# Optimization experiments

Hardware: AMD Instinct MI355X
Metric: run time of the kernel (lower is better)

Reference implementation:

```python
import jax, jax.numpy as jnp
import numpy as np

B, T, H = 8, 4096, 1024

def setup_inputs() -> dict:
    key = jax.random.key(0)
    k1, k2, k3, k4 = jax.random.split(key, 4)
    states = jax.random.normal(k1, (B, T, H), dtype=jnp.float32)
    context = jax.random.normal(k2, (B, H), dtype=jnp.float32)
    # nn.Bilinear(H, H, 1): weight (1, H, H), bias (1,), init U(-1/sqrt(H), 1/sqrt(H))
    bound = 1.0 / np.sqrt(H)
    W = jax.random.uniform(k3, (1, H, H), dtype=jnp.float32, minval=-bound, maxval=bound)
    b = jax.random.uniform(k4, (1,), dtype=jnp.float32, minval=-bound, maxval=bound)
    return {"states": states, "context": context, "W": W, "b": b}

def reference(states, context, W, b):
    # score[b,t,0] = sum_{i,j} states[b,t,i] * W[0,i,j] * context[b,j] + b[0]
    # Algebraic rewrite: v[b,i] = sum_j W[0,i,j] * context[b,j]; score = states @ v + b
    v = jnp.einsum('ij,bj->bi', W[0], context)          # (B, H)
    scores = jnp.einsum('bti,bi->bt', states, v) + b[0]  # (B, T)
    return scores[..., None]                             # (B, T, 1)
```

## Files before the change

kernel.cpp:

```cpp
#include <hip/hip_runtime.h>


#define HDIM 1024
#define BDIM 8
#define TDIM 4096

typedef float v4f __attribute__((ext_vector_type(4)));

__global__ __launch_bounds__(256) void gs_compute_v(
    const float* __restrict__ W,
    const float* __restrict__ ctx,
    float* __restrict__ v)
{
    const int wave = (blockIdx.x << 2) | (threadIdx.x >> 6);
    const int lane = threadIdx.x & 63;
    const int i = wave >> 3;
    const int b = wave & 7;

    const v4f* __restrict__ Wrow = (const v4f*)(W + (size_t)i * HDIM);
    const v4f* __restrict__ Crow = (const v4f*)(ctx + (size_t)b * HDIM);

    float acc = 0.0f;
#pragma unroll
    for (int k = 0; k < 4; ++k) {
        v4f w4 = Wrow[k * 64 + lane];
        v4f c4 = Crow[k * 64 + lane];
        acc += w4.x * c4.x + w4.y * c4.y + w4.z * c4.z + w4.w * c4.w;
    }
#pragma unroll
    for (int off = 32; off > 0; off >>= 1)
        acc += __shfl_down(acc, off, 64);

    if (lane == 0) v[b * HDIM + i] = acc;
}

__global__ __launch_bounds__(256) void gs_compute_scores(
    const float* __restrict__ states,
    const float* __restrict__ v,
    const float* __restrict__ bias,
    float* __restrict__ out)
{
    const int row = (blockIdx.x << 2) | (threadIdx.x >> 6);
    const int lane = threadIdx.x & 63;
    const int b = row >> 12;

    const v4f* __restrict__ Srow = (const v4f*)(states + (size_t)row * HDIM);
    const v4f* __restrict__ Vrow = (const v4f*)(v + (size_t)b * HDIM);

    float acc = 0.0f;
#pragma unroll
    for (int k = 0; k < 4; ++k) {
        v4f s4 = __builtin_nontemporal_load(&Srow[k * 64 + lane]);
        v4f v4 = Vrow[k * 64 + lane];
        acc += s4.x * v4.x + s4.y * v4.y + s4.z * v4.z + s4.w * v4.w;
    }
#pragma unroll
    for (int off = 32; off > 0; off >>= 1)
        acc += __shfl_down(acc, off, 64);

    if (lane == 0) out[row] = acc + bias[0];
}

extern "C" void kernel_launch(void* const* d_in, const int* in_sizes, int n_in,
                              void* d_out, int out_size, void* d_ws, size_t ws_size,
                              hipStream_t stream)
{
    const float* states = (const float*)d_in[0];
    const float* ctx    = (const float*)d_in[1];
    const float* W      = (const float*)d_in[2];
    const float* bias   = (const float*)d_in[3];
    float* out = (float*)d_out;
    float* v   = (float*)d_ws;

    gs_compute_v<<<dim3((BDIM * HDIM) / 4), dim3(256), 0, stream>>>(W, ctx, v);
    gs_compute_scores<<<dim3((BDIM * TDIM) / 4), dim3(256), 0, stream>>>(states, v, bias, out);
}
```

Baseline: 186.4 us.

## Reuse W rows across batches and process multiple state rows per wave

The v kernel now has each wave handle one W row for all eight batch entries. W is read once instead of once per batch, at the cost of eight accumulators per lane. The scores kernel makes each wave process four consecutive rows and keeps the v slice and bias in registers. This cuts redundant v loads and launches fewer blocks, with more independent loads in flight per wave.

Measured after the change: 189.7 us. About the same (+1.8%).

```diff
diff --git a/kernel.cpp b/kernel.cpp
--- a/kernel.cpp
+++ b/kernel.cpp
@@ -4,6 +4,7 @@
 #define HDIM 1024
 #define BDIM 8
 #define TDIM 4096
+#define RPW  4
 
 typedef float v4f __attribute__((ext_vector_type(4)));
 
@@ -14,24 +15,36 @@
 {
     const int wave = (blockIdx.x << 2) | (threadIdx.x >> 6);
     const int lane = threadIdx.x & 63;
-    const int i = wave >> 3;
-    const int b = wave & 7;
 
-    const v4f* __restrict__ Wrow = (const v4f*)(W + (size_t)i * HDIM);
-    const v4f* __restrict__ Crow = (const v4f*)(ctx + (size_t)b * HDIM);
+    const v4f* __restrict__ Wrow = (const v4f*)(W + (size_t)wave * HDIM);
+    const v4f* __restrict__ C    = (const v4f*)ctx;
 
-    float acc = 0.0f;
+    float acc[BDIM];
+#pragma unroll
+    for (int b = 0; b < BDIM; ++b) acc[b] = 0.0f;
+
 #pragma unroll
     for (int k = 0; k < 4; ++k) {
         v4f w4 = Wrow[k * 64 + lane];
-        v4f c4 = Crow[k * 64 + lane];
-        acc += w4.x * c4.x + w4.y * c4.y + w4.z * c4.z + w4.w * c4.w;
+#pragma unroll
+        for (int b = 0; b < BDIM; ++b) {
+            v4f c4 = C[b * (HDIM / 4) + k * 64 + lane];
+            acc[b] += w4.x * c4.x + w4.y * c4.y + w4.z * c4.z + w4.w * c4.w;
+        }
     }
+
 #pragma unroll
-    for (int off = 32; off > 0; off >>= 1)
-        acc += __shfl_down(acc, off, 64);
+    for (int b = 0; b < BDIM; ++b) {
+#pragma unroll
+        for (int off = 32; off > 0; off >>= 1)
+            acc[b] += __shfl_down(acc[b], off, 64);
+    }
 
-    if (lane == 0) v[b * HDIM + i] = acc;
+    if (lane == 0) {
+#pragma unroll
+        for (int b = 0; b < BDIM; ++b)
+            v[b * HDIM + wave] = acc[b];
+    }
 }
 
 __global__ __launch_bounds__(256) void gs_compute_scores(
@@ -40,25 +53,37 @@
     const float* __restrict__ bias,
     float* __restrict__ out)
 {
-    const int row = (blockIdx.x << 2) | (threadIdx.x >> 6);
+    const int wave = (blockIdx.x << 2) | (threadIdx.x >> 6);
     const int lane = threadIdx.x & 63;
-    const int b = row >> 12;
+    const int row0 = wave * RPW;
+    const int b = row0 >> 12;
 
-    const v4f* __restrict__ Srow = (const v4f*)(states + (size_t)row * HDIM);
-    const v4f* __restrict__ Vrow = (const v4f*)(v + (size_t)b * HDIM);
+    const v4f* __restrict__ V = (const v4f*)(v + (size_t)b * HDIM);
+    const v4f vr0 = V[0 * 64 + lane];
+    const v4f vr1 = V[1 * 64 + lane];
+    const v4f vr2 = V[2 * 64 + lane];
+    const v4f vr3 = V[3 * 64 + lane];
+    const float bb = bias[0];
 
-    float acc = 0.0f;
 #pragma unroll
-    for (int k = 0; k < 4; ++k) {
-        v4f s4 = __builtin_nontemporal_load(&Srow[k * 64 + lane]);
-        v4f v4 = Vrow[k * 64 + lane];
-        acc += s4.x * v4.x + s4.y * v4.y + s4.z * v4.z + s4.w * v4.w;
+    for (int r = 0; r < RPW; ++r) {
+        const v4f* __restrict__ S = (const v4f*)(states + (size_t)(row0 + r) * HDIM);
+        v4f s0 = __builtin_nontemporal_load(&S[0 * 64 + lane]);
+        v4f s1 = __builtin_nontemporal_load(&S[1 * 64 + lane]);
+        v4f s2 = __builtin_nontemporal_load(&S[2 * 64 + lane]);
+        v4f s3 = __builtin_nontemporal_load(&S[3 * 64 + lane]);
+
+        float acc = s0.x * vr0.x + s0.y * vr0.y + s0.z * vr0.z + s0.w * vr0.w;
+        acc      += s1.x * vr1.x + s1.y * vr1.y + s1.z * vr1.z + s1.w * vr1.w;
+        acc      += s2.x * vr2.x + s2.y * vr2.y + s2.z * vr2.z + s2.w * vr2.w;
+        acc      += s3.x * vr3.x + s3.y * vr3.y + s3.z * vr3.z + s3.w * vr3.w;
+
+#pragma unroll
+        for (int off = 32; off > 0; off >>= 1)
+            acc += __shfl_down(acc, off, 64);
+
+        if (lane == 0) out[row0 + r] = acc + bb;
     }
-#pragma unroll
-    for (int off = 32; off > 0; off >>= 1)
-        acc += __shfl_down(acc, off, 64);
-
-    if (lane == 0) out[row] = acc + bias[0];
 }
 
 extern "C" void kernel_launch(void* const* d_in, const int* in_sizes, int n_in,
@@ -72,6 +97,6 @@
     float* out = (float*)d_out;
     float* v   = (float*)d_ws;
 
-    gs_compute_v<<<dim3((BDIM * HDIM) / 4), dim3(256), 0, stream>>>(W, ctx, v);
-    gs_compute_scores<<<dim3((BDIM * TDIM) / 4), dim3(256), 0, stream>>>(states, v, bias, out);
+    gs_compute_v<<<dim3(HDIM / 4), dim3(256), 0, stream>>>(W, ctx, v);
+    gs_compute_scores<<<dim3((BDIM * TDIM) / (4 * RPW)), dim3(256), 0, stream>>>(states, v, bias, out);
 }
```
